# Performance work log

Hardware: AMD Instinct MI355X
Metric: run time of the kernel (lower is better)

## Reference

```python
import jax, jax.numpy as jnp
import numpy as np

RADIUS = 64
STRIDE = RADIUS // 2
EPS = 1e-5

def box_filter(x, w):
    # depthwise conv: groups=3, RADIUSxRADIUS kernel of ones, stride RADIUS//2, no padding
    return jax.lax.conv_general_dilated(
        x, w, window_strides=(STRIDE, STRIDE), padding='VALID',
        feature_group_count=3, dimension_numbers=('NCHW', 'OIHW', 'NCHW'))

def conv1x1(x, w):
    # 1x1 conv == per-pixel matmul over channels
    return jnp.einsum('bchw,oc->bohw', x, w)

def batchnorm(x, g, b):
    # BatchNorm2d in training mode: biased batch stats over (N,H,W)
    m = jnp.mean(x, axis=(0, 2, 3), keepdims=True)
    v = jnp.var(x, axis=(0, 2, 3), keepdims=True)
    return (x - m) * jax.lax.rsqrt(v + EPS) * g[None, :, None, None] + b[None, :, None, None]

def resize_bilinear_ac(x, oh, ow):
    # F.interpolate(mode='bilinear', align_corners=True), separable gathers
    B, C, h, w = x.shape
    ys = jnp.linspace(0.0, h - 1.0, oh)
    y0 = jnp.floor(ys).astype(jnp.int32)
    y1 = jnp.minimum(y0 + 1, h - 1)
    wy = (ys - y0.astype(x.dtype))[None, None, :, None]
    xh = jnp.take(x, y0, axis=2) * (1 - wy) + jnp.take(x, y1, axis=2) * wy
    xs = jnp.linspace(0.0, w - 1.0, ow)
    x0 = jnp.floor(xs).astype(jnp.int32)
    x1 = jnp.minimum(x0 + 1, w - 1)
    wx = (xs - x0.astype(x.dtype))[None, None, None, :]
    return jnp.take(xh, x0, axis=3) * (1 - wx) + jnp.take(xh, x1, axis=3) * wx

def setup_inputs():
    key = jax.random.key(0)
    ks = jax.random.split(key, 5)
    B, H, W = 4, 1024, 1024
    guide = jax.random.uniform(ks[0], (B, 3, H, W), dtype=jnp.float32)
    src = jax.random.uniform(ks[1], (B, 3, H, W), dtype=jnp.float32)
    box_w = jnp.ones((3, 1, RADIUS, RADIUS), jnp.float32)  # weight.data[...] = 1.0
    w1 = jax.random.normal(ks[2], (32, 6), jnp.float32) * 0.2
    w2 = jax.random.normal(ks[3], (32, 32), jnp.float32) * 0.2
    w3 = jax.random.normal(ks[4], (3, 32), jnp.float32) * 0.2
    g1 = jnp.ones((32,), jnp.float32); b1 = jnp.zeros((32,), jnp.float32)
    g2 = jnp.ones((32,), jnp.float32); b2 = jnp.zeros((32,), jnp.float32)
    return dict(guide=guide, src=src, box_w=box_w, w1=w1, g1=g1, b1=b1,
                w2=w2, g2=g2, b2=b2, w3=w3)

def reference(guide, src, box_w, w1, g1, b1, w2, g2, b2, w3):
    B, C, H, W = guide.shape
    N = box_filter(jnp.ones((1, 3, H, W), guide.dtype), box_w)  # local window counts
    mean_x = box_filter(guide, box_w) / N
    mean_y = box_filter(src, box_w) / N
    cov_xy = box_filter(guide * src, box_w) / N - mean_x * mean_y
    var_x = box_filter(guide * guide, box_w) / N - mean_x * mean_x
    h = jnp.concatenate([cov_xy, var_x], axis=1)  # [B,6,h',w']
    h = jax.nn.relu(batchnorm(conv1x1(h, w1), g1, b1))
    h = jax.nn.relu(batchnorm(conv1x1(h, w2), g2, b2))
    A = conv1x1(h, w3)  # [B,3,h',w']
    b = mean_y - A * mean_x
    mean_A = resize_bilinear_ac(A, H, W)
    mean_b = resize_bilinear_ac(b, H, W)
    return mean_A * guide + mean_b
```

## Files before the change

kernel.cpp:

```cpp
#include <hip/hip_runtime.h>
#include <stdint.h>

#define B_      4
#define C_      3
#define H_      1024
#define W_      1024
#define OH_     31
#define NHS_    64
#define NP_     3844
#define NPOSPB_ 961
#define EPS_    1e-5f

#define NBLK_MID 16

#define TILE_PLANE 24576
#define OFF_TILE  0
#define OFF_STATS 98304
#define OFF_BAR   98432
#define OFF_A     98436
#define OFF_BV    109968

typedef float f4 __attribute__((ext_vector_type(4)));

__global__ __launch_bounds__(256) void k1_tilesums(
        const float* __restrict__ g,
        const float* __restrict__ s,
        float* __restrict__ ws) {
    int blk = blockIdx.x;
    int bc = blk >> 6;
    int hs = blk & 63;
    int t  = threadIdx.x;
    const f4* gp = (const f4*)(g + ((size_t)bc * H_ + (size_t)hs * 16) * W_);
    const f4* sp = (const f4*)(s + ((size_t)bc * H_ + (size_t)hs * 16) * W_);
    float sg = 0.f, ss = 0.f, sgs = 0.f, sgg = 0.f;
#pragma unroll 4
    for (int r = 0; r < 16; r++) {
        f4 gv = gp[r * (W_ / 4) + t];
        f4 sv = __builtin_nontemporal_load(sp + r * (W_ / 4) + t);
        sg  += (gv.x + gv.y) + (gv.z + gv.w);
        ss  += (sv.x + sv.y) + (sv.z + sv.w);
        sgs += gv.x * sv.x + gv.y * sv.y + gv.z * sv.z + gv.w * sv.w;
        sgg += gv.x * gv.x + gv.y * gv.y + gv.z * gv.z + gv.w * gv.w;
    }
#pragma unroll
    for (int off = 4; off; off >>= 1) {
        sg  += __shfl_down(sg,  off, 8);
        ss  += __shfl_down(ss,  off, 8);
        sgs += __shfl_down(sgs, off, 8);
        sgg += __shfl_down(sgg, off, 8);
    }
    if ((t & 7) == 0) {
        int tx = t >> 3;
        int base = (bc * NHS_ + hs) * 32 + tx;
        ws[OFF_TILE + 0 * TILE_PLANE + base] = sg;
        ws[OFF_TILE + 1 * TILE_PLANE + base] = ss;
        ws[OFF_TILE + 2 * TILE_PLANE + base] = sgs;
        ws[OFF_TILE + 3 * TILE_PLANE + base] = sgg;
    }
    if (blk == 0 && t < 132) ws[OFF_STATS + t] = 0.f;
}

__device__ __forceinline__ void bar16(float* ws, int idx) {
    __syncthreads();
    if (threadIdx.x == 0) {
        __threadfence();
        int* ctr = (int*)(ws + OFF_BAR) + idx;
        __atomic_fetch_add(ctr, 1, __ATOMIC_ACQ_REL);
        while (__hip_atomic_load(ctr, __ATOMIC_ACQUIRE, __HIP_MEMORY_SCOPE_AGENT) < NBLK_MID) {
            __builtin_amdgcn_s_sleep(1);
        }
    }
    __syncthreads();
}

__global__ __launch_bounds__(1024) void kmid(
        const float* __restrict__ w1f,
        const float* __restrict__ g1f,
        const float* __restrict__ b1f,
        const float* __restrict__ w2f,
        const float* __restrict__ g2f,
        const float* __restrict__ b2f,
        const float* __restrict__ w3f,
        float* __restrict__ ws) {
    __shared__ float zbuf[256 * 33];
    __shared__ float red[16][16];
    __shared__ float scs[32], shs[32];
    int t    = threadIdx.x;
    int w    = t >> 6;
    int lane = t & 63;
    int k    = w & 3;
    int ko8  = __builtin_amdgcn_readfirstlane(k * 8);
    int pl   = (w >> 2) * 64 + lane;
    int p    = blockIdx.x * 256 + pl;
    bool ok  = p < NP_;
    int pp   = ok ? p : 0;
    int b    = pp / NPOSPB_;
    int r    = pp % NPOSPB_;
    int oy   = r / OH_, ox = r % OH_;

    float h[6], mxv[3], myv[3];
#pragma unroll
    for (int c = 0; c < 3; c++) {
        int bc = b * 3 + c;
        int base = (bc * NHS_ + oy * 2) * 32 + ox;
        float S[4];
#pragma unroll
        for (int plane = 0; plane < 4; plane++) {
            const float* tp = ws + OFF_TILE + plane * TILE_PLANE + base;
            S[plane] = ((tp[0]  + tp[1])  + (tp[32] + tp[33]))
                     + ((tp[64] + tp[65]) + (tp[96] + tp[97]));
        }
        const float inv = 1.f / 4096.f;
        float mx = S[0] * inv, my = S[1] * inv;
        h[c]     = S[2] * inv - mx * my;
        h[3 + c] = S[3] * inv - mx * mx;
        mxv[c] = mx; myv[c] = my;
    }
    float a[8];
#pragma unroll
    for (int j = 0; j < 8; j++) {
        float y = 0.f;
#pragma unroll
        for (int i = 0; i < 6; i++) y += w1f[(ko8 + j) * 6 + i] * h[i];
        a[j] = y;
    }

    {
        float sv[8], sq[8];
#pragma unroll
        for (int j = 0; j < 8; j++) { sv[j] = ok ? a[j] : 0.f; sq[j] = sv[j] * sv[j]; }
#pragma unroll
        for (int off = 32; off; off >>= 1) {
#pragma unroll
            for (int j = 0; j < 8; j++) {
                sv[j] += __shfl_down(sv[j], off, 64);
                sq[j] += __shfl_down(sq[j], off, 64);
            }
        }
        if (lane == 0) {
#pragma unroll
            for (int j = 0; j < 8; j++) { red[w][j] = sv[j]; red[w][8 + j] = sq[j]; }
        }
    }
    __syncthreads();
    if (t < 64) {
        int o = t & 31; int kk = o >> 3; int col = ((t >= 32) ? 8 : 0) + (o & 7);
        float tot = red[kk][col] + red[kk + 4][col] + red[kk + 8][col] + red[kk + 12][col];
        atomicAdd(&ws[OFF_STATS + ((t >= 32) ? 32 : 0) + o], tot);
    }
    bar16(ws, 0);

    if (t < 32) {
        float sm = __hip_atomic_load(&ws[OFF_STATS + t],      __ATOMIC_RELAXED, __HIP_MEMORY_SCOPE_AGENT);
        float sq = __hip_atomic_load(&ws[OFF_STATS + 32 + t], __ATOMIC_RELAXED, __HIP_MEMORY_SCOPE_AGENT);
        float m = sm * (1.f / NP_);
        float v = sq * (1.f / NP_) - m * m;
        float sc = g1f[t] * rsqrtf(v + EPS_);
        scs[t] = sc; shs[t] = b1f[t] - m * sc;
    }
    __syncthreads();

#pragma unroll
    for (int j = 0; j < 8; j++) {
        float zz = fmaxf(a[j] * scs[ko8 + j] + shs[ko8 + j], 0.f);
        zbuf[pl * 33 + ko8 + j] = zz;
    }
    __syncthreads();
    float zal[32];
#pragma unroll
    for (int i = 0; i < 32; i++) zal[i] = zbuf[pl * 33 + i];
    float y2[8];
#pragma unroll
    for (int j = 0; j < 8; j++) {
        float y = 0.f;
#pragma unroll
        for (int i = 0; i < 32; i++) y += w2f[(ko8 + j) * 32 + i] * zal[i];
        y2[j] = y;
    }

    {
        float sv[8], sq[8];
#pragma unroll
        for (int j = 0; j < 8; j++) { sv[j] = ok ? y2[j] : 0.f; sq[j] = sv[j] * sv[j]; }
#pragma unroll
        for (int off = 32; off; off >>= 1) {
#pragma unroll
            for (int j = 0; j < 8; j++) {
                sv[j] += __shfl_down(sv[j], off, 64);
                sq[j] += __shfl_down(sq[j], off, 64);
            }
        }
        if (lane == 0) {
#pragma unroll
            for (int j = 0; j < 8; j++) { red[w][j] = sv[j]; red[w][8 + j] = sq[j]; }
        }
    }
    __syncthreads();
    if (t < 64) {
        int o = t & 31; int kk = o >> 3; int col = ((t >= 32) ? 8 : 0) + (o & 7);
        float tot = red[kk][col] + red[kk + 4][col] + red[kk + 8][col] + red[kk + 12][col];
        atomicAdd(&ws[OFF_STATS + 64 + ((t >= 32) ? 32 : 0) + o], tot);
    }
    bar16(ws, 1);

    if (t < 32) {
        float sm = __hip_atomic_load(&ws[OFF_STATS + 64 + t], __ATOMIC_RELAXED, __HIP_MEMORY_SCOPE_AGENT);
        float sq = __hip_atomic_load(&ws[OFF_STATS + 96 + t], __ATOMIC_RELAXED, __HIP_MEMORY_SCOPE_AGENT);
        float m = sm * (1.f / NP_);
        float v = sq * (1.f / NP_) - m * m;
        float sc = g2f[t] * rsqrtf(v + EPS_);
        scs[t] = sc; shs[t] = b2f[t] - m * sc;
    }
    __syncthreads();

#pragma unroll
    for (int j = 0; j < 8; j++) {
        float zz = fmaxf(y2[j] * scs[ko8 + j] + shs[ko8 + j], 0.f);
        zbuf[pl * 33 + ko8 + j] = zz;
    }
    __syncthreads();
    if (k == 0 && ok) {
        float z2[32];
#pragma unroll
        for (int i = 0; i < 32; i++) z2[i] = zbuf[pl * 33 + i];
#pragma unroll
        for (int c = 0; c < 3; c++) {
            float av = 0.f;
#pragma unroll
            for (int i = 0; i < 32; i++) av += w3f[c * 32 + i] * z2[i];
            ws[OFF_A  + c * NP_ + p] = av;
            ws[OFF_BV + c * NP_ + p] = myv[c] - av * mxv[c];
        }
    }
}

__global__ __launch_bounds__(256) void k5_final(
        const float* __restrict__ g,
        const float* __restrict__ ws,
        float* __restrict__ out) {
    int blk = blockIdx.x;
    int y  = blk & 1023;
    int bc = blk >> 10;
    int b = bc / 3, c = bc % 3;
    float fy = (float)y * (30.f / 1023.f);
    int y0 = (int)fy;
    float wy = fy - (float)y0;
    int y1i = min(y0 + 1, 30);
    const float* A0 = ws + OFF_A  + c * NP_ + b * NPOSPB_ + y0  * OH_;
    const float* A1 = ws + OFF_A  + c * NP_ + b * NPOSPB_ + y1i * OH_;
    const float* B0 = ws + OFF_BV + c * NP_ + b * NPOSPB_ + y0  * OH_;
    const float* B1 = ws + OFF_BV + c * NP_ + b * NPOSPB_ + y1i * OH_;
    int t = threadIdx.x;
    size_t rowoff = ((size_t)bc * H_ + (size_t)y) * W_;
    const f4* gp = (const f4*)(g + rowoff);
    f4* op = (f4*)(out + rowoff);
    f4 gv = gp[t];
    float go[4] = { gv.x, gv.y, gv.z, gv.w };
    float r[4];
#pragma unroll
    for (int j = 0; j < 4; j++) {
        int x = t * 4 + j;
        float fx = (float)x * (30.f / 1023.f);
        int x0 = (int)fx;
        float wx = fx - (float)x0;
        int x1 = min(x0 + 1, 30);
        float a  = (A0[x0] * (1.f - wx) + A0[x1] * wx) * (1.f - wy)
                 + (A1[x0] * (1.f - wx) + A1[x1] * wx) * wy;
        float bb = (B0[x0] * (1.f - wx) + B0[x1] * wx) * (1.f - wy)
                 + (B1[x0] * (1.f - wx) + B1[x1] * wx) * wy;
        r[j] = a * go[j] + bb;
    }
    f4 ov;
    ov.x = r[0]; ov.y = r[1]; ov.z = r[2]; ov.w = r[3];
    __builtin_nontemporal_store(ov, op + t);
}

extern "C" void kernel_launch(void* const* d_in, const int* in_sizes, int n_in,
                              void* d_out, int out_size, void* d_ws, size_t ws_size,
                              hipStream_t stream) {
    const float* guide = (const float*)d_in[0];
    const float* src   = (const float*)d_in[1];
    const float* w1 = (const float*)d_in[3];
    const float* g1 = (const float*)d_in[4];
    const float* b1 = (const float*)d_in[5];
    const float* w2 = (const float*)d_in[6];
    const float* g2 = (const float*)d_in[7];
    const float* b2 = (const float*)d_in[8];
    const float* w3 = (const float*)d_in[9];
    float* ws = (float*)d_ws;
    float* out = (float*)d_out;

    hipLaunchKernelGGL(k1_tilesums, dim3(B_ * C_ * NHS_), dim3(256),  0, stream, guide, src, ws);
    hipLaunchKernelGGL(kmid,        dim3(NBLK_MID),       dim3(1024), 0, stream,
                       w1, g1, b1, w2, g2, b2, w3, ws);
    hipLaunchKernelGGL(k5_final,    dim3(B_ * C_ * H_),   dim3(256),  0, stream, guide, ws, out);
}
```

Baseline: 181.8 us.

## Fuse three kernels into one cooperative persistent kernel with global barriers

Merges the tile-sum, MLP/batchnorm and final upsample kernels into a single cooperative launch of 192 blocks of 1024 threads. Stage boundaries are enforced with device-global atomic counters, and a last-block reset re-arms them for the next call. This removes two kernel launch gaps and the per-launch tail effects. In exchange, the 176 non-mid blocks idle-spin while 16 blocks do the serial MLP stage, and the final stage now runs with far fewer threads (16 rows per 256-thread group) than the old 12288-block launch, which may reduce memory-level parallelism.

Measured after the change: 512.2 us. +181.8%, slower.

```diff
diff --git a/kernel.cpp b/kernel.cpp
--- a/kernel.cpp
+++ b/kernel.cpp
@@ -11,7 +11,8 @@
 #define NPOSPB_ 961
 #define EPS_    1e-5f
 
-#define NBLK_MID 16
+#define NBLK_    192
+#define MIDBLK_  16
 
 #define TILE_PLANE 24576
 #define OFF_TILE  0
@@ -21,6 +22,290 @@
 #define OFF_BV    109968
 
 typedef float f4 __attribute__((ext_vector_type(4)));
+
+__device__ int g_bar[8];
+
+#define BLK_RELEASE_ARRIVE(idx) do { \
+    __threadfence(); __syncthreads(); \
+    if (t == 0) __atomic_fetch_add(&g_bar[idx], 1, __ATOMIC_ACQ_REL); \
+} while (0)
+#define BLK_WAIT(idx, target) do { \
+    if (t == 0) { \
+        while (__hip_atomic_load(&g_bar[idx], __ATOMIC_ACQUIRE, __HIP_MEMORY_SCOPE_AGENT) < (target)) \
+            __builtin_amdgcn_s_sleep(1); \
+    } \
+    __syncthreads(); \
+} while (0)
+
+__global__ __launch_bounds__(1024) void fused(
+        const float* __restrict__ g,
+        const float* __restrict__ s,
+        const float* __restrict__ w1f,
+        const float* __restrict__ g1f,
+        const float* __restrict__ b1f,
+        const float* __restrict__ w2f,
+        const float* __restrict__ g2f,
+        const float* __restrict__ b2f,
+        const float* __restrict__ w3f,
+        float* __restrict__ ws,
+        float* __restrict__ out) {
+    __shared__ float zbuf[256 * 33];
+    __shared__ float red[16][16];
+    __shared__ float scs[32], shs[32];
+    int t  = threadIdx.x;
+    int fb = blockIdx.x;
+
+    {
+        int sub = t >> 8;
+        int st  = t & 255;
+        int blk = fb * 4 + sub;
+        int bc = blk >> 6;
+        int hs = blk & 63;
+        const f4* gp = (const f4*)(g + ((size_t)bc * H_ + (size_t)hs * 16) * W_);
+        const f4* sp = (const f4*)(s + ((size_t)bc * H_ + (size_t)hs * 16) * W_);
+        float sg = 0.f, ss = 0.f, sgs = 0.f, sgg = 0.f;
+#pragma unroll 4
+        for (int r = 0; r < 16; r++) {
+            f4 gv = gp[r * (W_ / 4) + st];
+            f4 sv = __builtin_nontemporal_load(sp + r * (W_ / 4) + st);
+            sg  += (gv.x + gv.y) + (gv.z + gv.w);
+            ss  += (sv.x + sv.y) + (sv.z + sv.w);
+            sgs += gv.x * sv.x + gv.y * sv.y + gv.z * sv.z + gv.w * sv.w;
+            sgg += gv.x * gv.x + gv.y * gv.y + gv.z * gv.z + gv.w * gv.w;
+        }
+#pragma unroll
+        for (int off = 4; off; off >>= 1) {
+            sg  += __shfl_down(sg,  off, 8);
+            ss  += __shfl_down(ss,  off, 8);
+            sgs += __shfl_down(sgs, off, 8);
+            sgg += __shfl_down(sgg, off, 8);
+        }
+        if ((st & 7) == 0) {
+            int tx = st >> 3;
+            int base = (bc * NHS_ + hs) * 32 + tx;
+            ws[OFF_TILE + 0 * TILE_PLANE + base] = sg;
+            ws[OFF_TILE + 1 * TILE_PLANE + base] = ss;
+            ws[OFF_TILE + 2 * TILE_PLANE + base] = sgs;
+            ws[OFF_TILE + 3 * TILE_PLANE + base] = sgg;
+        }
+        if (fb == 0 && t < 128) ws[OFF_STATS + t] = 0.f;
+    }
+    BLK_RELEASE_ARRIVE(0);
+
+    if (fb < MIDBLK_) {
+        BLK_WAIT(0, NBLK_);
+
+        int w    = t >> 6;
+        int lane = t & 63;
+        int k    = w & 3;
+        int ko8  = __builtin_amdgcn_readfirstlane(k * 8);
+        int pl   = (w >> 2) * 64 + lane;
+        int p    = fb * 256 + pl;
+        bool ok  = p < NP_;
+        int pp   = ok ? p : 0;
+        int b    = pp / NPOSPB_;
+        int r    = pp % NPOSPB_;
+        int oy   = r / OH_, ox = r % OH_;
+
+        float h[6], mxv[3], myv[3];
+#pragma unroll
+        for (int c = 0; c < 3; c++) {
+            int bc = b * 3 + c;
+            int base = (bc * NHS_ + oy * 2) * 32 + ox;
+            float S[4];
+#pragma unroll
+            for (int plane = 0; plane < 4; plane++) {
+                const float* tp = ws + OFF_TILE + plane * TILE_PLANE + base;
+                S[plane] = ((tp[0]  + tp[1])  + (tp[32] + tp[33]))
+                         + ((tp[64] + tp[65]) + (tp[96] + tp[97]));
+            }
+            const float inv = 1.f / 4096.f;
+            float mx = S[0] * inv, my = S[1] * inv;
+            h[c]     = S[2] * inv - mx * my;
+            h[3 + c] = S[3] * inv - mx * mx;
+            mxv[c] = mx; myv[c] = my;
+        }
+        float a[8];
+#pragma unroll
+        for (int j = 0; j < 8; j++) {
+            float y = 0.f;
+#pragma unroll
+            for (int i = 0; i < 6; i++) y += w1f[(ko8 + j) * 6 + i] * h[i];
+            a[j] = y;
+        }
+
+        {
+            float sv[8], sq[8];
+#pragma unroll
+            for (int j = 0; j < 8; j++) { sv[j] = ok ? a[j] : 0.f; sq[j] = sv[j] * sv[j]; }
+#pragma unroll
+            for (int off = 32; off; off >>= 1) {
+#pragma unroll
+                for (int j = 0; j < 8; j++) {
+                    sv[j] += __shfl_down(sv[j], off, 64);
+                    sq[j] += __shfl_down(sq[j], off, 64);
+                }
+            }
+            if (lane == 0) {
+#pragma unroll
+                for (int j = 0; j < 8; j++) { red[w][j] = sv[j]; red[w][8 + j] = sq[j]; }
+            }
+        }
+        __syncthreads();
+        if (t < 64) {
+            int o = t & 31; int kk = o >> 3; int col = ((t >= 32) ? 8 : 0) + (o & 7);
+            float tot = red[kk][col] + red[kk + 4][col] + red[kk + 8][col] + red[kk + 12][col];
+            atomicAdd(&ws[OFF_STATS + ((t >= 32) ? 32 : 0) + o], tot);
+        }
+        BLK_RELEASE_ARRIVE(1);
+        BLK_WAIT(1, MIDBLK_);
+
+        if (t < 32) {
+            float sm = __hip_atomic_load(&ws[OFF_STATS + t],      __ATOMIC_RELAXED, __HIP_MEMORY_SCOPE_AGENT);
+            float sq = __hip_atomic_load(&ws[OFF_STATS + 32 + t], __ATOMIC_RELAXED, __HIP_MEMORY_SCOPE_AGENT);
+            float m = sm * (1.f / NP_);
+            float v = sq * (1.f / NP_) - m * m;
+            float sc = g1f[t] * rsqrtf(v + EPS_);
+            scs[t] = sc; shs[t] = b1f[t] - m * sc;
+        }
+        __syncthreads();
+
+#pragma unroll
+        for (int j = 0; j < 8; j++) {
+            float zz = fmaxf(a[j] * scs[ko8 + j] + shs[ko8 + j], 0.f);
+            zbuf[pl * 33 + ko8 + j] = zz;
+        }
+        __syncthreads();
+        float zal[32];
+#pragma unroll
+        for (int i = 0; i < 32; i++) zal[i] = zbuf[pl * 33 + i];
+        float y2[8];
+#pragma unroll
+        for (int j = 0; j < 8; j++) {
+            float y = 0.f;
+#pragma unroll
+            for (int i = 0; i < 32; i++) y += w2f[(ko8 + j) * 32 + i] * zal[i];
+            y2[j] = y;
+        }
+
+        {
+            float sv[8], sq[8];
+#pragma unroll
+            for (int j = 0; j < 8; j++) { sv[j] = ok ? y2[j] : 0.f; sq[j] = sv[j] * sv[j]; }
+#pragma unroll
+            for (int off = 32; off; off >>= 1) {
+#pragma unroll
+                for (int j = 0; j < 8; j++) {
+                    sv[j] += __shfl_down(sv[j], off, 64);
+                    sq[j] += __shfl_down(sq[j], off, 64);
+                }
+            }
+            if (lane == 0) {
+#pragma unroll
+                for (int j = 0; j < 8; j++) { red[w][j] = sv[j]; red[w][8 + j] = sq[j]; }
+            }
+        }
+        __syncthreads();
+        if (t < 64) {
+            int o = t & 31; int kk = o >> 3; int col = ((t >= 32) ? 8 : 0) + (o & 7);
+            float tot = red[kk][col] + red[kk + 4][col] + red[kk + 8][col] + red[kk + 12][col];
+            atomicAdd(&ws[OFF_STATS + 64 + ((t >= 32) ? 32 : 0) + o], tot);
+        }
+        BLK_RELEASE_ARRIVE(2);
+        BLK_WAIT(2, MIDBLK_);
+
+        if (t < 32) {
+            float sm = __hip_atomic_load(&ws[OFF_STATS + 64 + t], __ATOMIC_RELAXED, __HIP_MEMORY_SCOPE_AGENT);
+            float sq = __hip_atomic_load(&ws[OFF_STATS + 96 + t], __ATOMIC_RELAXED, __HIP_MEMORY_SCOPE_AGENT);
+            float m = sm * (1.f / NP_);
+            float v = sq * (1.f / NP_) - m * m;
+            float sc = g2f[t] * rsqrtf(v + EPS_);
+            scs[t] = sc; shs[t] = b2f[t] - m * sc;
+        }
+        __syncthreads();
+
+#pragma unroll
+        for (int j = 0; j < 8; j++) {
+            float zz = fmaxf(y2[j] * scs[ko8 + j] + shs[ko8 + j], 0.f);
+            zbuf[pl * 33 + ko8 + j] = zz;
+        }
+        __syncthreads();
+        if (k == 0 && ok) {
+            float z2[32];
+#pragma unroll
+            for (int i = 0; i < 32; i++) z2[i] = zbuf[pl * 33 + i];
+#pragma unroll
+            for (int c = 0; c < 3; c++) {
+                float av = 0.f;
+#pragma unroll
+                for (int i = 0; i < 32; i++) av += w3f[c * 32 + i] * z2[i];
+                ws[OFF_A  + c * NP_ + p] = av;
+                ws[OFF_BV + c * NP_ + p] = myv[c] - av * mxv[c];
+            }
+        }
+        BLK_RELEASE_ARRIVE(3);
+        BLK_WAIT(3, MIDBLK_);
+    } else {
+        BLK_WAIT(3, MIDBLK_);
+    }
+
+    {
+        int sub = t >> 8;
+        int st  = t & 255;
+        int row0 = fb * 64 + sub * 16;
+        int bc = row0 >> 10;
+        int b5 = bc / 3, c5 = bc % 3;
+        const float* Abase = ws + OFF_A  + c5 * NP_ + b5 * NPOSPB_;
+        const float* Bbase = ws + OFF_BV + c5 * NP_ + b5 * NPOSPB_;
+        int x0_[4], x1_[4]; float wx_[4];
+#pragma unroll
+        for (int j = 0; j < 4; j++) {
+            int x = st * 4 + j;
+            float fx = (float)x * (30.f / 1023.f);
+            int x0 = (int)fx;
+            wx_[j] = fx - (float)x0;
+            x0_[j] = x0;
+            x1_[j] = min(x0 + 1, 30);
+        }
+        for (int rr = 0; rr < 16; rr++) {
+            int y = (row0 & 1023) + rr;
+            float fy = (float)y * (30.f / 1023.f);
+            int y0 = (int)fy;
+            float wy = fy - (float)y0;
+            int y1i = min(y0 + 1, 30);
+            const float* A0 = Abase + y0  * OH_;
+            const float* A1 = Abase + y1i * OH_;
+            const float* B0 = Bbase + y0  * OH_;
+            const float* B1 = Bbase + y1i * OH_;
+            size_t rowoff = ((size_t)bc * H_ + (size_t)y) * W_;
+            f4 gv = ((const f4*)(g + rowoff))[st];
+            float go[4] = { gv.x, gv.y, gv.z, gv.w };
+            float r[4];
+#pragma unroll
+            for (int j = 0; j < 4; j++) {
+                int x0 = x0_[j], x1 = x1_[j];
+                float wx = wx_[j];
+                float av = (A0[x0] * (1.f - wx) + A0[x1] * wx) * (1.f - wy)
+                         + (A1[x0] * (1.f - wx) + A1[x1] * wx) * wy;
+                float bb = (B0[x0] * (1.f - wx) + B0[x1] * wx) * (1.f - wy)
+                         + (B1[x0] * (1.f - wx) + B1[x1] * wx) * wy;
+                r[j] = av * go[j] + bb;
+            }
+            f4 ov; ov.x = r[0]; ov.y = r[1]; ov.z = r[2]; ov.w = r[3];
+            __builtin_nontemporal_store(ov, (f4*)(out + rowoff) + st);
+        }
+    }
+
+    __syncthreads();
+    if (t == 0) {
+        int old = __atomic_fetch_add(&g_bar[4], 1, __ATOMIC_ACQ_REL);
+        if (old == NBLK_ - 1) {
+            g_bar[0] = 0; g_bar[1] = 0; g_bar[2] = 0; g_bar[3] = 0;
+            __threadfence();
+            g_bar[4] = 0;
+        }
+    }
+}
 
 __global__ __launch_bounds__(256) void k1_tilesums(
         const float* __restrict__ g,
@@ -66,7 +351,7 @@
         __threadfence();
         int* ctr = (int*)(ws + OFF_BAR) + idx;
         __atomic_fetch_add(ctr, 1, __ATOMIC_ACQ_REL);
-        while (__hip_atomic_load(ctr, __ATOMIC_ACQUIRE, __HIP_MEMORY_SCOPE_AGENT) < NBLK_MID) {
+        while (__hip_atomic_load(ctr, __ATOMIC_ACQUIRE, __HIP_MEMORY_SCOPE_AGENT) < MIDBLK_) {
             __builtin_amdgcn_s_sleep(1);
         }
     }
@@ -124,7 +409,6 @@
         for (int i = 0; i < 6; i++) y += w1f[(ko8 + j) * 6 + i] * h[i];
         a[j] = y;
     }
-
     {
         float sv[8], sq[8];
 #pragma unroll
@@ -149,7 +433,6 @@
         atomicAdd(&ws[OFF_STATS + ((t >= 32) ? 32 : 0) + o], tot);
     }
     bar16(ws, 0);
-
     if (t < 32) {
         float sm = __hip_atomic_load(&ws[OFF_STATS + t],      __ATOMIC_RELAXED, __HIP_MEMORY_SCOPE_AGENT);
         float sq = __hip_atomic_load(&ws[OFF_STATS + 32 + t], __ATOMIC_RELAXED, __HIP_MEMORY_SCOPE_AGENT);
@@ -159,7 +442,6 @@
         scs[t] = sc; shs[t] = b1f[t] - m * sc;
     }
     __syncthreads();
-
 #pragma unroll
     for (int j = 0; j < 8; j++) {
         float zz = fmaxf(a[j] * scs[ko8 + j] + shs[ko8 + j], 0.f);
@@ -177,7 +459,6 @@
         for (int i = 0; i < 32; i++) y += w2f[(ko8 + j) * 32 + i] * zal[i];
         y2[j] = y;
     }
-
     {
         float sv[8], sq[8];
 #pragma unroll
@@ -202,7 +483,6 @@
         atomicAdd(&ws[OFF_STATS + 64 + ((t >= 32) ? 32 : 0) + o], tot);
     }
     bar16(ws, 1);
-
     if (t < 32) {
         float sm = __hip_atomic_load(&ws[OFF_STATS + 64 + t], __ATOMIC_RELAXED, __HIP_MEMORY_SCOPE_AGENT);
         float sq = __hip_atomic_load(&ws[OFF_STATS + 96 + t], __ATOMIC_RELAXED, __HIP_MEMORY_SCOPE_AGENT);
@@ -212,7 +492,6 @@
         scs[t] = sc; shs[t] = b2f[t] - m * sc;
     }
     __syncthreads();
-
 #pragma unroll
     for (int j = 0; j < 8; j++) {
         float zz = fmaxf(y2[j] * scs[ko8 + j] + shs[ko8 + j], 0.f);
@@ -290,8 +569,16 @@
     float* ws = (float*)d_ws;
     float* out = (float*)d_out;
 
-    hipLaunchKernelGGL(k1_tilesums, dim3(B_ * C_ * NHS_), dim3(256),  0, stream, guide, src, ws);
-    hipLaunchKernelGGL(kmid,        dim3(NBLK_MID),       dim3(1024), 0, stream,
-                       w1, g1, b1, w2, g2, b2, w3, ws);
-    hipLaunchKernelGGL(k5_final,    dim3(B_ * C_ * H_),   dim3(256),  0, stream, guide, ws, out);
+    void* args[] = { (void*)&guide, (void*)&src,
+                     (void*)&w1, (void*)&g1, (void*)&b1,
+                     (void*)&w2, (void*)&g2, (void*)&b2, (void*)&w3,
+                     (void*)&ws, (void*)&out };
+    hipError_t e = hipLaunchCooperativeKernel((const void*)fused,
+                                              dim3(NBLK_), dim3(1024), args, 0, stream);
+    if (e != hipSuccess) {
+        hipLaunchKernelGGL(k1_tilesums, dim3(B_ * C_ * NHS_), dim3(256),  0, stream, guide, src, ws);
+        hipLaunchKernelGGL(kmid,        dim3(MIDBLK_),        dim3(1024), 0, stream,
+                           w1, g1, b1, w2, g2, b2, w3, ws);
+        hipLaunchKernelGGL(k5_final,    dim3(B_ * C_ * H_),   dim3(256),  0, stream, guide, ws, out);
+    }
 }
```

## Fuse three kernels into one persistent kernel with sharded grid barriers

Applied to the files above, without the earlier changes.

Merges the tile-sum, MLP/batchnorm, and final upsample kernels into one persistent 192-block kernel. Blocks signal completion of the tile-sum phase through sharded atomic counters, 16 blocks run the MLP with their own BN barriers, and all blocks spin-wait before writing output. A parity flip resets the counters for the next call. This removes two kernel launch gaps, but the final phase now runs on only 192 blocks that each loop over 16 rows. It also assumes all 192 blocks of 1024 threads are co-resident, otherwise the spin-waits deadlock.

New measurement: 233.7 us. 1.29x slower.

```diff
diff --git a/kernel.cpp b/kernel.cpp
--- a/kernel.cpp
+++ b/kernel.cpp
@@ -11,69 +11,36 @@
 #define NPOSPB_ 961
 #define EPS_    1e-5f
 
-#define NBLK_MID 16
+#define NBLK_    192
+#define MIDBLK_  16
+#define NSHARD_  8
+#define SHARD_TGT_ 24
+#define LINE_    32
 
 #define TILE_PLANE 24576
 #define OFF_TILE  0
 #define OFF_STATS 98304
-#define OFF_BAR   98432
-#define OFF_A     98436
-#define OFF_BV    109968
+#define OFF_A     98432
+#define OFF_BV    109964
 
 typedef float f4 __attribute__((ext_vector_type(4)));
 
-__global__ __launch_bounds__(256) void k1_tilesums(
+__device__ int g_shard[2][NSHARD_ * LINE_];
+__device__ int g_root[2][LINE_];
+__device__ int g_bn1[2][LINE_];
+__device__ int g_bn2[2][LINE_];
+__device__ int g_done[2][LINE_];
+__device__ int g_parity;
+
+static __device__ __forceinline__ int  aload(int* p)  { return __hip_atomic_load(p, __ATOMIC_ACQUIRE, __HIP_MEMORY_SCOPE_AGENT); }
+static __device__ __forceinline__ int  aadd(int* p, int v) { return __hip_atomic_fetch_add(p, v, __ATOMIC_ACQ_REL, __HIP_MEMORY_SCOPE_AGENT); }
+static __device__ __forceinline__ void astoref(float* p, float v) { __hip_atomic_store(p, v, __ATOMIC_RELAXED, __HIP_MEMORY_SCOPE_AGENT); }
+static __device__ __forceinline__ void astorei(int* p, int v)     { __hip_atomic_store(p, v, __ATOMIC_RELAXED, __HIP_MEMORY_SCOPE_AGENT); }
+static __device__ __forceinline__ float aloadf(float* p) { return __hip_atomic_load(p, __ATOMIC_RELAXED, __HIP_MEMORY_SCOPE_AGENT); }
+
+__global__ __launch_bounds__(1024) void fused(
         const float* __restrict__ g,
         const float* __restrict__ s,
-        float* __restrict__ ws) {
-    int blk = blockIdx.x;
-    int bc = blk >> 6;
-    int hs = blk & 63;
-    int t  = threadIdx.x;
-    const f4* gp = (const f4*)(g + ((size_t)bc * H_ + (size_t)hs * 16) * W_);
-    const f4* sp = (const f4*)(s + ((size_t)bc * H_ + (size_t)hs * 16) * W_);
-    float sg = 0.f, ss = 0.f, sgs = 0.f, sgg = 0.f;
-#pragma unroll 4
-    for (int r = 0; r < 16; r++) {
-        f4 gv = gp[r * (W_ / 4) + t];
-        f4 sv = __builtin_nontemporal_load(sp + r * (W_ / 4) + t);
-        sg  += (gv.x + gv.y) + (gv.z + gv.w);
-        ss  += (sv.x + sv.y) + (sv.z + sv.w);
-        sgs += gv.x * sv.x + gv.y * sv.y + gv.z * sv.z + gv.w * sv.w;
-        sgg += gv.x * gv.x + gv.y * gv.y + gv.z * gv.z + gv.w * gv.w;
-    }
-#pragma unroll
-    for (int off = 4; off; off >>= 1) {
-        sg  += __shfl_down(sg,  off, 8);
-        ss  += __shfl_down(ss,  off, 8);
-        sgs += __shfl_down(sgs, off, 8);
-        sgg += __shfl_down(sgg, off, 8);
-    }
-    if ((t & 7) == 0) {
-        int tx = t >> 3;
-        int base = (bc * NHS_ + hs) * 32 + tx;
-        ws[OFF_TILE + 0 * TILE_PLANE + base] = sg;
-        ws[OFF_TILE + 1 * TILE_PLANE + base] = ss;
-        ws[OFF_TILE + 2 * TILE_PLANE + base] = sgs;
-        ws[OFF_TILE + 3 * TILE_PLANE + base] = sgg;
-    }
-    if (blk == 0 && t < 132) ws[OFF_STATS + t] = 0.f;
-}
-
-__device__ __forceinline__ void bar16(float* ws, int idx) {
-    __syncthreads();
-    if (threadIdx.x == 0) {
-        __threadfence();
-        int* ctr = (int*)(ws + OFF_BAR) + idx;
-        __atomic_fetch_add(ctr, 1, __ATOMIC_ACQ_REL);
-        while (__hip_atomic_load(ctr, __ATOMIC_ACQUIRE, __HIP_MEMORY_SCOPE_AGENT) < NBLK_MID) {
-            __builtin_amdgcn_s_sleep(1);
-        }
-    }
-    __syncthreads();
-}
-
-__global__ __launch_bounds__(1024) void kmid(
         const float* __restrict__ w1f,
         const float* __restrict__ g1f,
         const float* __restrict__ b1f,
@@ -81,198 +48,285 @@
         const float* __restrict__ g2f,
         const float* __restrict__ b2f,
         const float* __restrict__ w3f,
-        float* __restrict__ ws) {
+        float* __restrict__ ws,
+        float* __restrict__ out) {
     __shared__ float zbuf[256 * 33];
     __shared__ float red[16][16];
     __shared__ float scs[32], shs[32];
-    int t    = threadIdx.x;
-    int w    = t >> 6;
-    int lane = t & 63;
-    int k    = w & 3;
-    int ko8  = __builtin_amdgcn_readfirstlane(k * 8);
-    int pl   = (w >> 2) * 64 + lane;
-    int p    = blockIdx.x * 256 + pl;
-    bool ok  = p < NP_;
-    int pp   = ok ? p : 0;
-    int b    = pp / NPOSPB_;
-    int r    = pp % NPOSPB_;
-    int oy   = r / OH_, ox = r % OH_;
-
-    float h[6], mxv[3], myv[3];
-#pragma unroll
-    for (int c = 0; c < 3; c++) {
-        int bc = b * 3 + c;
-        int base = (bc * NHS_ + oy * 2) * 32 + ox;
-        float S[4];
-#pragma unroll
-        for (int plane = 0; plane < 4; plane++) {
-            const float* tp = ws + OFF_TILE + plane * TILE_PLANE + base;
-            S[plane] = ((tp[0]  + tp[1])  + (tp[32] + tp[33]))
-                     + ((tp[64] + tp[65]) + (tp[96] + tp[97]));
-        }
-        const float inv = 1.f / 4096.f;
-        float mx = S[0] * inv, my = S[1] * inv;
-        h[c]     = S[2] * inv - mx * my;
-        h[3 + c] = S[3] * inv - mx * mx;
-        mxv[c] = mx; myv[c] = my;
-    }
-    float a[8];
-#pragma unroll
-    for (int j = 0; j < 8; j++) {
-        float y = 0.f;
-#pragma unroll
-        for (int i = 0; i < 6; i++) y += w1f[(ko8 + j) * 6 + i] * h[i];
-        a[j] = y;
-    }
+    __shared__ int sP;
+    int t  = threadIdx.x;
+    int fb = blockIdx.x;
+    if (t == 0) sP = __hip_atomic_load(&g_parity, __ATOMIC_RELAXED, __HIP_MEMORY_SCOPE_AGENT);
 
     {
-        float sv[8], sq[8];
-#pragma unroll
-        for (int j = 0; j < 8; j++) { sv[j] = ok ? a[j] : 0.f; sq[j] = sv[j] * sv[j]; }
-#pragma unroll
-        for (int off = 32; off; off >>= 1) {
-#pragma unroll
-            for (int j = 0; j < 8; j++) {
-                sv[j] += __shfl_down(sv[j], off, 64);
-                sq[j] += __shfl_down(sq[j], off, 64);
-            }
-        }
-        if (lane == 0) {
-#pragma unroll
-            for (int j = 0; j < 8; j++) { red[w][j] = sv[j]; red[w][8 + j] = sq[j]; }
-        }
+        int sub = t >> 8;
+        int st  = t & 255;
+        int blk = fb * 4 + sub;
+        int bc = blk >> 6;
+        int hs = blk & 63;
+        const f4* gp = (const f4*)(g + ((size_t)bc * H_ + (size_t)hs * 16) * W_);
+        const f4* sp = (const f4*)(s + ((size_t)bc * H_ + (size_t)hs * 16) * W_);
+        float sg = 0.f, ss = 0.f, sgs = 0.f, sgg = 0.f;
+#pragma unroll 4
+        for (int r = 0; r < 16; r++) {
+            f4 gv = gp[r * (W_ / 4) + st];
+            f4 sv = __builtin_nontemporal_load(sp + r * (W_ / 4) + st);
+            sg  += (gv.x + gv.y) + (gv.z + gv.w);
+            ss  += (sv.x + sv.y) + (sv.z + sv.w);
+            sgs += gv.x * sv.x + gv.y * sv.y + gv.z * sv.z + gv.w * sv.w;
+            sgg += gv.x * gv.x + gv.y * gv.y + gv.z * gv.z + gv.w * gv.w;
+        }
+#pragma unroll
+        for (int off = 4; off; off >>= 1) {
+            sg  += __shfl_down(sg,  off, 8);
+            ss  += __shfl_down(ss,  off, 8);
+            sgs += __shfl_down(sgs, off, 8);
+            sgg += __shfl_down(sgg, off, 8);
+        }
+        if ((st & 7) == 0) {
+            int tx = st >> 3;
+            int base = (bc * NHS_ + hs) * 32 + tx;
+            astoref(&ws[OFF_TILE + 0 * TILE_PLANE + base], sg);
+            astoref(&ws[OFF_TILE + 1 * TILE_PLANE + base], ss);
+            astoref(&ws[OFF_TILE + 2 * TILE_PLANE + base], sgs);
+            astoref(&ws[OFF_TILE + 3 * TILE_PLANE + base], sgg);
+        }
+        if (fb == 0 && t < 128) astoref(&ws[OFF_STATS + t], 0.f);
     }
     __syncthreads();
-    if (t < 64) {
-        int o = t & 31; int kk = o >> 3; int col = ((t >= 32) ? 8 : 0) + (o & 7);
-        float tot = red[kk][col] + red[kk + 4][col] + red[kk + 8][col] + red[kk + 12][col];
-        atomicAdd(&ws[OFF_STATS + ((t >= 32) ? 32 : 0) + o], tot);
+    int P = sP;
+
+    if (t == 0) {
+        int sh = fb & (NSHARD_ - 1);
+        int old = aadd(&g_shard[P][sh * LINE_], 1);
+        if (old == SHARD_TGT_ - 1) aadd(&g_root[P][0], 1);
     }
-    bar16(ws, 0);
-
-    if (t < 32) {
-        float sm = __hip_atomic_load(&ws[OFF_STATS + t],      __ATOMIC_RELAXED, __HIP_MEMORY_SCOPE_AGENT);
-        float sq = __hip_atomic_load(&ws[OFF_STATS + 32 + t], __ATOMIC_RELAXED, __HIP_MEMORY_SCOPE_AGENT);
-        float m = sm * (1.f / NP_);
-        float v = sq * (1.f / NP_) - m * m;
-        float sc = g1f[t] * rsqrtf(v + EPS_);
-        scs[t] = sc; shs[t] = b1f[t] - m * sc;
+
+    if (fb < MIDBLK_) {
+        if (t == 0) { while (aload(&g_root[P][0]) < NSHARD_) __builtin_amdgcn_s_sleep(8); }
+        __syncthreads();
+
+        int w    = t >> 6;
+        int lane = t & 63;
+        int k    = w & 3;
+        int ko8  = __builtin_amdgcn_readfirstlane(k * 8);
+        int pl   = (w >> 2) * 64 + lane;
+        int p    = fb * 256 + pl;
+        bool ok  = p < NP_;
+        int pp   = ok ? p : 0;
+        int b    = pp / NPOSPB_;
+        int r    = pp % NPOSPB_;
+        int oy   = r / OH_, ox = r % OH_;
+
+        float h[6], mxv[3], myv[3];
+#pragma unroll
+        for (int c = 0; c < 3; c++) {
+            int bc = b * 3 + c;
+            int base = (bc * NHS_ + oy * 2) * 32 + ox;
+            float S[4];
+#pragma unroll
+            for (int plane = 0; plane < 4; plane++) {
+                const float* tp = ws + OFF_TILE + plane * TILE_PLANE + base;
+                S[plane] = ((tp[0]  + tp[1])  + (tp[32] + tp[33]))
+                         + ((tp[64] + tp[65]) + (tp[96] + tp[97]));
+            }
+            const float inv = 1.f / 4096.f;
+            float mx = S[0] * inv, my = S[1] * inv;
+            h[c]     = S[2] * inv - mx * my;
+            h[3 + c] = S[3] * inv - mx * mx;
+            mxv[c] = mx; myv[c] = my;
+        }
+        float a[8];
+#pragma unroll
+        for (int j = 0; j < 8; j++) {
+            float y = 0.f;
+#pragma unroll
+            for (int i = 0; i < 6; i++) y += w1f[(ko8 + j) * 6 + i] * h[i];
+            a[j] = y;
+        }
+
+        {
+            float sv[8], sq[8];
+#pragma unroll
+            for (int j = 0; j < 8; j++) { sv[j] = ok ? a[j] : 0.f; sq[j] = sv[j] * sv[j]; }
+#pragma unroll
+            for (int off = 32; off; off >>= 1) {
+#pragma unroll
+                for (int j = 0; j < 8; j++) {
+                    sv[j] += __shfl_down(sv[j], off, 64);
+                    sq[j] += __shfl_down(sq[j], off, 64);
+                }
+            }
+            if (lane == 0) {
+#pragma unroll
+                for (int j = 0; j < 8; j++) { red[w][j] = sv[j]; red[w][8 + j] = sq[j]; }
+            }
+        }
+        __syncthreads();
+        if (t < 64) {
+            int o = t & 31; int kk = o >> 3; int col = ((t >= 32) ? 8 : 0) + (o & 7);
+            float tot = red[kk][col] + red[kk + 4][col] + red[kk + 8][col] + red[kk + 12][col];
+            atomicAdd(&ws[OFF_STATS + ((t >= 32) ? 32 : 0) + o], tot);
+        }
+        __syncthreads();
+        if (t == 0) {
+            aadd(&g_bn1[P][0], 1);
+            while (aload(&g_bn1[P][0]) < MIDBLK_) __builtin_amdgcn_s_sleep(8);
+        }
+        __syncthreads();
+
+        if (t < 32) {
+            float sm = aloadf(&ws[OFF_STATS + t]);
+            float sq = aloadf(&ws[OFF_STATS + 32 + t]);
+            float m = sm * (1.f / NP_);
+            float v = sq * (1.f / NP_) - m * m;
+            float sc = g1f[t] * rsqrtf(v + EPS_);
+            scs[t] = sc; shs[t] = b1f[t] - m * sc;
+        }
+        __syncthreads();
+
+#pragma unroll
+        for (int j = 0; j < 8; j++) {
+            float zz = fmaxf(a[j] * scs[ko8 + j] + shs[ko8 + j], 0.f);
+            zbuf[pl * 33 + ko8 + j] = zz;
+        }
+        __syncthreads();
+        float zal[32];
+#pragma unroll
+        for (int i = 0; i < 32; i++) zal[i] = zbuf[pl * 33 + i];
+        float y2[8];
+#pragma unroll
+        for (int j = 0; j < 8; j++) {
+            float y = 0.f;
+#pragma unroll
+            for (int i = 0; i < 32; i++) y += w2f[(ko8 + j) * 32 + i] * zal[i];
+            y2[j] = y;
+        }
+
+        {
+            float sv[8], sq[8];
+#pragma unroll
+            for (int j = 0; j < 8; j++) { sv[j] = ok ? y2[j] : 0.f; sq[j] = sv[j] * sv[j]; }
+#pragma unroll
+            for (int off = 32; off; off >>= 1) {
+#pragma unroll
+                for (int j = 0; j < 8; j++) {
+                    sv[j] += __shfl_down(sv[j], off, 64);
+                    sq[j] += __shfl_down(sq[j], off, 64);
+                }
+            }
+            if (lane == 0) {
+#pragma unroll
+                for (int j = 0; j < 8; j++) { red[w][j] = sv[j]; red[w][8 + j] = sq[j]; }
+            }
+        }
+        __syncthreads();
+        if (t < 64) {
+            int o = t & 31; int kk = o >> 3; int col = ((t >= 32) ? 8 : 0) + (o & 7);
+            float tot = red[kk][col] + red[kk + 4][col] + red[kk + 8][col] + red[kk + 12][col];
+            atomicAdd(&ws[OFF_STATS + 64 + ((t >= 32) ? 32 : 0) + o], tot);
+        }
+        __syncthreads();
+        if (t == 0) {
+            aadd(&g_bn2[P][0], 1);
+            while (aload(&g_bn2[P][0]) < MIDBLK_) __builtin_amdgcn_s_sleep(8);
+        }
+        __syncthreads();
+
+        if (t < 32) {
+            float sm = aloadf(&ws[OFF_STATS + 64 + t]);
+            float sq = aloadf(&ws[OFF_STATS + 96 + t]);
+            float m = sm * (1.f / NP_);
+            float v = sq * (1.f / NP_) - m * m;
+            float sc = g2f[t] * rsqrtf(v + EPS_);
+            scs[t] = sc; shs[t] = b2f[t] - m * sc;
+        }
+        __syncthreads();
+
+#pragma unroll
+        for (int j = 0; j < 8; j++) {
+            float zz = fmaxf(y2[j] * scs[ko8 + j] + shs[ko8 + j], 0.f);
+            zbuf[pl * 33 + ko8 + j] = zz;
+        }
+        __syncthreads();
+        if (k == 0 && ok) {
+            float z2[32];
+#pragma unroll
+            for (int i = 0; i < 32; i++) z2[i] = zbuf[pl * 33 + i];
+#pragma unroll
+            for (int c = 0; c < 3; c++) {
+                float av = 0.f;
+#pragma unroll
+                for (int i = 0; i < 32; i++) av += w3f[c * 32 + i] * z2[i];
+                astoref(&ws[OFF_A  + c * NP_ + p], av);
+                astoref(&ws[OFF_BV + c * NP_ + p], myv[c] - av * mxv[c]);
+            }
+        }
+        __syncthreads();
+        if (t == 0) {
+            int old = aadd(&g_done[P][0], 1);
+            if (old == MIDBLK_ - 1) {
+                int Q = P ^ 1;
+#pragma unroll
+                for (int i = 0; i < NSHARD_; i++) astorei(&g_shard[Q][i * LINE_], 0);
+                astorei(&g_root[Q][0], 0);
+                astorei(&g_bn1[Q][0], 0);
+                astorei(&g_bn2[Q][0], 0);
+                astorei(&g_done[Q][0], 0);
+                __hip_atomic_store(&g_parity, Q, __ATOMIC_RELEASE, __HIP_MEMORY_SCOPE_AGENT);
+            }
+        }
     }
+
+    if (t == 0) { while (aload(&g_done[P][0]) < MIDBLK_) __builtin_amdgcn_s_sleep(16); }
     __syncthreads();
 
-#pragma unroll
-    for (int j = 0; j < 8; j++) {
-        float zz = fmaxf(a[j] * scs[ko8 + j] + shs[ko8 + j], 0.f);
-        zbuf[pl * 33 + ko8 + j] = zz;
+    {
+        int sub = t >> 8;
+        int st  = t & 255;
+        int row0 = fb * 64 + sub * 16;
+        int bc = row0 >> 10;
+        int b5 = bc / 3, c5 = bc % 3;
+        const float* Abase = ws + OFF_A  + c5 * NP_ + b5 * NPOSPB_;
+        const float* Bbase = ws + OFF_BV + c5 * NP_ + b5 * NPOSPB_;
+        int x0_[4], x1_[4]; float wx_[4];
+#pragma unroll
+        for (int j = 0; j < 4; j++) {
+            int x = st * 4 + j;
+            float fx = (float)x * (30.f / 1023.f);
+            int x0 = (int)fx;
+            wx_[j] = fx - (float)x0;
+            x0_[j] = x0;
+            x1_[j] = min(x0 + 1, 30);
+        }
+        for (int rr = 0; rr < 16; rr++) {
+            int y = (row0 & 1023) + rr;
+            float fy = (float)y * (30.f / 1023.f);
+            int y0 = (int)fy;
+            float wy = fy - (float)y0;
+            int y1i = min(y0 + 1, 30);
+            const float* A0 = Abase + y0  * OH_;
+            const float* A1 = Abase + y1i * OH_;
+            const float* B0 = Bbase + y0  * OH_;
+            const float* B1 = Bbase + y1i * OH_;
+            size_t rowoff = ((size_t)bc * H_ + (size_t)y) * W_;
+            f4 gv = ((const f4*)(g + rowoff))[st];
+            float go[4] = { gv.x, gv.y, gv.z, gv.w };
+            float r[4];
+#pragma unroll
+            for (int j = 0; j < 4; j++) {
+                int x0 = x0_[j], x1 = x1_[j];
+                float wx = wx_[j];
+                float av = (A0[x0] * (1.f - wx) + A0[x1] * wx) * (1.f - wy)
+                         + (A1[x0] * (1.f - wx) + A1[x1] * wx) * wy;
+                float bb = (B0[x0] * (1.f - wx) + B0[x1] * wx) * (1.f - wy)
+                         + (B1[x0] * (1.f - wx) + B1[x1] * wx) * wy;
+                r[j] = av * go[j] + bb;
+            }
+            f4 ov; ov.x = r[0]; ov.y = r[1]; ov.z = r[2]; ov.w = r[3];
+            __builtin_nontemporal_store(ov, (f4*)(out + rowoff) + st);
+        }
     }
-    __syncthreads();
-    float zal[32];
-#pragma unroll
-    for (int i = 0; i < 32; i++) zal[i] = zbuf[pl * 33 + i];
-    float y2[8];
-#pragma unroll
-    for (int j = 0; j < 8; j++) {
-        float y = 0.f;
-#pragma unroll
-        for (int i = 0; i < 32; i++) y += w2f[(ko8 + j) * 32 + i] * zal[i];
-        y2[j] = y;
-    }
-
-    {
-        float sv[8], sq[8];
-#pragma unroll
-        for (int j = 0; j < 8; j++) { sv[j] = ok ? y2[j] : 0.f; sq[j] = sv[j] * sv[j]; }
-#pragma unroll
-        for (int off = 32; off; off >>= 1) {
-#pragma unroll
-            for (int j = 0; j < 8; j++) {
-                sv[j] += __shfl_down(sv[j], off, 64);
-                sq[j] += __shfl_down(sq[j], off, 64);
-            }
-        }
-        if (lane == 0) {
-#pragma unroll
-            for (int j = 0; j < 8; j++) { red[w][j] = sv[j]; red[w][8 + j] = sq[j]; }
-        }
-    }
-    __syncthreads();
-    if (t < 64) {
-        int o = t & 31; int kk = o >> 3; int col = ((t >= 32) ? 8 : 0) + (o & 7);
-        float tot = red[kk][col] + red[kk + 4][col] + red[kk + 8][col] + red[kk + 12][col];
-        atomicAdd(&ws[OFF_STATS + 64 + ((t >= 32) ? 32 : 0) + o], tot);
-    }
-    bar16(ws, 1);
-
-    if (t < 32) {
-        float sm = __hip_atomic_load(&ws[OFF_STATS + 64 + t], __ATOMIC_RELAXED, __HIP_MEMORY_SCOPE_AGENT);
-        float sq = __hip_atomic_load(&ws[OFF_STATS + 96 + t], __ATOMIC_RELAXED, __HIP_MEMORY_SCOPE_AGENT);
-        float m = sm * (1.f / NP_);
-        float v = sq * (1.f / NP_) - m * m;
-        float sc = g2f[t] * rsqrtf(v + EPS_);
-        scs[t] = sc; shs[t] = b2f[t] - m * sc;
-    }
-    __syncthreads();
-
-#pragma unroll
-    for (int j = 0; j < 8; j++) {
-        float zz = fmaxf(y2[j] * scs[ko8 + j] + shs[ko8 + j], 0.f);
-        zbuf[pl * 33 + ko8 + j] = zz;
-    }
-    __syncthreads();
-    if (k == 0 && ok) {
-        float z2[32];
-#pragma unroll
-        for (int i = 0; i < 32; i++) z2[i] = zbuf[pl * 33 + i];
-#pragma unroll
-        for (int c = 0; c < 3; c++) {
-            float av = 0.f;
-#pragma unroll
-            for (int i = 0; i < 32; i++) av += w3f[c * 32 + i] * z2[i];
-            ws[OFF_A  + c * NP_ + p] = av;
-            ws[OFF_BV + c * NP_ + p] = myv[c] - av * mxv[c];
-        }
-    }
-}
-
-__global__ __launch_bounds__(256) void k5_final(
-        const float* __restrict__ g,
-        const float* __restrict__ ws,
-        float* __restrict__ out) {
-    int blk = blockIdx.x;
-    int y  = blk & 1023;
-    int bc = blk >> 10;
-    int b = bc / 3, c = bc % 3;
-    float fy = (float)y * (30.f / 1023.f);
-    int y0 = (int)fy;
-    float wy = fy - (float)y0;
-    int y1i = min(y0 + 1, 30);
-    const float* A0 = ws + OFF_A  + c * NP_ + b * NPOSPB_ + y0  * OH_;
-    const float* A1 = ws + OFF_A  + c * NP_ + b * NPOSPB_ + y1i * OH_;
-    const float* B0 = ws + OFF_BV + c * NP_ + b * NPOSPB_ + y0  * OH_;
-    const float* B1 = ws + OFF_BV + c * NP_ + b * NPOSPB_ + y1i * OH_;
-    int t = threadIdx.x;
-    size_t rowoff = ((size_t)bc * H_ + (size_t)y) * W_;
-    const f4* gp = (const f4*)(g + rowoff);
-    f4* op = (f4*)(out + rowoff);
-    f4 gv = gp[t];
-    float go[4] = { gv.x, gv.y, gv.z, gv.w };
-    float r[4];
-#pragma unroll
-    for (int j = 0; j < 4; j++) {
-        int x = t * 4 + j;
-        float fx = (float)x * (30.f / 1023.f);
-        int x0 = (int)fx;
-        float wx = fx - (float)x0;
-        int x1 = min(x0 + 1, 30);
-        float a  = (A0[x0] * (1.f - wx) + A0[x1] * wx) * (1.f - wy)
-                 + (A1[x0] * (1.f - wx) + A1[x1] * wx) * wy;
-        float bb = (B0[x0] * (1.f - wx) + B0[x1] * wx) * (1.f - wy)
-                 + (B1[x0] * (1.f - wx) + B1[x1] * wx) * wy;
-        r[j] = a * go[j] + bb;
-    }
-    f4 ov;
-    ov.x = r[0]; ov.y = r[1]; ov.z = r[2]; ov.w = r[3];
-    __builtin_nontemporal_store(ov, op + t);
 }
 
 extern "C" void kernel_launch(void* const* d_in, const int* in_sizes, int n_in,
@@ -290,8 +344,6 @@
     float* ws = (float*)d_ws;
     float* out = (float*)d_out;
 
-    hipLaunchKernelGGL(k1_tilesums, dim3(B_ * C_ * NHS_), dim3(256),  0, stream, guide, src, ws);
-    hipLaunchKernelGGL(kmid,        dim3(NBLK_MID),       dim3(1024), 0, stream,
-                       w1, g1, b1, w2, g2, b2, w3, ws);
-    hipLaunchKernelGGL(k5_final,    dim3(B_ * C_ * H_),   dim3(256),  0, stream, guide, ws, out);
+    hipLaunchKernelGGL(fused, dim3(NBLK_), dim3(1024), 0, stream,
+                       guide, src, w1, g1, b1, w2, g2, b2, w3, ws, out);
 }
```
